# Kernel optimization log

Hardware: AMD Instinct MI355X
Metric: run time of the kernel (lower is better)

The kernel has to match this reference:

```python
import jax, jax.numpy as jnp
import numpy as np

B, V, P, L, D = 8, 16, 128, 16, 128
PD = L * D  # patch_dim = patch_size * d_model = 2048


def _layernorm(x, g, b, eps=1e-5):
    mu = jnp.mean(x, axis=-1, keepdims=True)
    var = jnp.mean(jnp.square(x - mu), axis=-1, keepdims=True)
    return (x - mu) / jnp.sqrt(var + eps) * g + b


def setup_inputs() -> dict:
    key = jax.random.key(0)
    ks = jax.random.split(key, 24)
    x = jax.random.normal(ks[0], (B, V, P, L, D), jnp.float32)
    m = jax.random.randint(ks[1], (B, V, V), 0, 2) > 0
    var_mask = m & ~jnp.eye(V, dtype=bool)[None]  # keep self-attention unmasked

    def lin_w(k, fan_in, fan_out):
        return jax.random.normal(k, (fan_in, fan_out), jnp.float32) * (1.0 / np.sqrt(fan_in))

    inp = {"x": x, "var_mask": var_mask}
    # Attn_PatchLevel (attn1): query / shared kv / out projections
    inp["w_q1"] = lin_w(ks[2], PD, PD); inp["b_q1"] = jnp.zeros((PD,), jnp.float32)
    inp["w_kv1"] = lin_w(ks[3], PD, PD); inp["b_kv1"] = jnp.zeros((PD,), jnp.float32)
    inp["w_o1"] = lin_w(ks[4], PD, PD); inp["b_o1"] = jnp.zeros((PD,), jnp.float32)
    # Attn_VarLevel (attn2)
    inp["w_q2"] = lin_w(ks[5], PD, PD); inp["b_q2"] = jnp.zeros((PD,), jnp.float32)
    inp["w_kv2"] = lin_w(ks[6], PD, PD); inp["b_kv2"] = jnp.zeros((PD,), jnp.float32)
    inp["w_o2"] = lin_w(ks[7], PD, PD); inp["b_o2"] = jnp.zeros((PD,), jnp.float32)
    # LayerNorms
    inp["g1"] = jnp.ones((PD,), jnp.float32); inp["be1"] = jnp.zeros((PD,), jnp.float32)
    inp["g2"] = jnp.ones((PD,), jnp.float32); inp["be2"] = jnp.zeros((PD,), jnp.float32)
    inp["g3"] = jnp.ones((PD,), jnp.float32); inp["be3"] = jnp.zeros((PD,), jnp.float32)
    # FFN
    inp["w_l1"] = lin_w(ks[8], PD, 4 * PD); inp["b_l1"] = jnp.zeros((4 * PD,), jnp.float32)
    inp["w_l2"] = lin_w(ks[9], 4 * PD, PD); inp["b_l2"] = jnp.zeros((PD,), jnp.float32)
    return inp


def reference(x, var_mask,
              w_q1, b_q1, w_kv1, b_kv1, w_o1, b_o1,
              w_q2, b_q2, w_kv2, b_kv2, w_o2, b_o2,
              g1, be1, g2, be2, g3, be3,
              w_l1, b_l1, w_l2, b_l2):
    b, v, p, l, d = x.shape
    pd = l * d
    scale = 1.0 / np.sqrt(pd)
    x = x.reshape(b, v, p, pd)

    # ---- Attn_PatchLevel (mask=None -> no masking; keys and values share kv_projection) ----
    q = x @ w_q1 + b_q1
    kv = x @ w_kv1 + b_kv1  # keys == values in the original module
    scores = jnp.einsum('bvpd,bvsd->bvps', q, kv)  # [B,V,P,P]
    attn = jax.nn.softmax(scale * scores, axis=-1)  # dropout is identity at eval
    a1 = jnp.einsum('bvps,bvsd->bvpd', attn, kv) @ w_o1 + b_o1
    x = _layernorm(x + a1, g1, be1)

    # ---- Attn_VarLevel over variables, per patch ----
    x = x.transpose(0, 2, 1, 3)  # [B,P,V,PD]
    q = x @ w_q2 + b_q2
    kv = x @ w_kv2 + b_kv2
    scores = jnp.einsum('bpvd,bprd->bpvr', q, kv)  # [B,P,V,V]
    scores = jnp.where(var_mask[:, None, :, :], -jnp.inf, scores)
    attn = jax.nn.softmax(scale * scores, axis=-1)
    a2 = jnp.einsum('bpvr,bprd->bpvd', attn, kv) @ w_o2 + b_o2
    x = _layernorm(x + a2, g2, be2)

    # ---- FFN (torch nn.GELU default = exact erf) ----
    z = jax.nn.gelu(x @ w_l1 + b_l1, approximate=False)
    x = x + z @ w_l2 + b_l2

    x_out = _layernorm(x, g3, be3).transpose(0, 2, 1, 3)  # [B,V,P,PD]
    x_next = x_out.reshape(b, v, p // 2, 2 * l, d)
    return x_out, x_next
```

## Files before the change

### kernel.cpp

```cpp
#include <hip/hip_runtime.h>
#include <math.h>


using u16   = unsigned short;
using f32x4 = __attribute__((ext_vector_type(4))) float;
using bf16x8= __attribute__((ext_vector_type(8))) __bf16;
using u16x8 = __attribute__((ext_vector_type(8))) u16;
using u16x4 = __attribute__((ext_vector_type(4))) u16;

#define NROWS 16384
#define PD    2048

__device__ __forceinline__ float bf2f(u16 u) {
    unsigned v = ((unsigned)u) << 16;
    return __builtin_bit_cast(float, v);
}
__device__ __forceinline__ u16 f2bf(float f) {
    unsigned u = __builtin_bit_cast(unsigned, f);
    u += 0x7FFFu + ((u >> 16) & 1u);
    return (u16)(u >> 16);
}
__device__ __forceinline__ void gload_lds16(const void* g, void* l) {
    __builtin_amdgcn_global_load_lds((const __attribute__((address_space(1))) void*)g,
                                     (__attribute__((address_space(3))) void*)l, 16, 0, 0);
}

template<int OUTF32, int GELU, int HASBIAS>
__global__ __launch_bounds__(256, 2)
void gemm_nt(const u16* __restrict__ A, long sAg, int lda,
             const u16* __restrict__ B, long sBg, int ldb,
             void* __restrict__ Cv, long sCg, int ldc,
             const float* __restrict__ bias, int K, float scale)
{
    __shared__ __align__(16) u16 lsA[128 * 32];
    __shared__ __align__(16) u16 lsB[128 * 32];

    const int tid  = threadIdx.x;
    const int w    = tid >> 6;
    const int lane = tid & 63;
    const int m0   = blockIdx.x * 128;
    const int n0   = blockIdx.y * 128;
    A += (long)blockIdx.z * sAg;
    B += (long)blockIdx.z * sBg;

    const int wr = w >> 1, wc = w & 1;

    f32x4 acc[4][4] = {};

    const int srow = lane >> 2;
    const int skc  = (lane & 3) * 8;
    const int rA0  = 32 * w + srow;
    const int rA1  = rA0 + 16;
    const size_t aoff0 = (size_t)(m0 + rA0) * lda + skc;
    const size_t aoff1 = (size_t)(m0 + rA1) * lda + skc;
    const size_t boff0 = (size_t)(n0 + rA0) * ldb + skc;
    const size_t boff1 = (size_t)(n0 + rA1) * ldb + skc;
    u16* lA0 = lsA + 1024 * w;
    u16* lA1 = lA0 + 512;
    u16* lB0 = lsB + 1024 * w;
    u16* lB1 = lB0 + 512;

    const int fr = lane & 15;
    const int fk = (lane >> 4) * 8;

    for (int k0 = 0; k0 < K; k0 += 32) {
        gload_lds16(A + aoff0 + k0, lA0);
        gload_lds16(A + aoff1 + k0, lA1);
        gload_lds16(B + boff0 + k0, lB0);
        gload_lds16(B + boff1 + k0, lB1);
        __syncthreads();

        bf16x8 af[4], bf[4];
        #pragma unroll
        for (int m = 0; m < 4; m++)
            af[m] = *(const bf16x8*)&lsA[(wr * 64 + m * 16 + fr) * 32 + fk];
        #pragma unroll
        for (int n = 0; n < 4; n++)
            bf[n] = *(const bf16x8*)&lsB[(wc * 64 + n * 16 + fr) * 32 + fk];
        #pragma unroll
        for (int m = 0; m < 4; m++)
            #pragma unroll
            for (int n = 0; n < 4; n++)
                acc[m][n] = __builtin_amdgcn_mfma_f32_16x16x32_bf16(af[m], bf[n], acc[m][n], 0, 0, 0);
        __syncthreads();
    }

    float* Cf = (float*)Cv;
    u16*   Cb = (u16*)Cv;
    const int crow0 = m0 + wr * 64 + (lane >> 4) * 4;
    const int ccol0 = n0 + wc * 64 + fr;
    const long cbase = (long)blockIdx.z * sCg;
    #pragma unroll
    for (int n = 0; n < 4; n++) {
        const int col = ccol0 + n * 16;
        float bb = 0.f;
        if constexpr (HASBIAS) bb = bias[col];
        #pragma unroll
        for (int m = 0; m < 4; m++) {
            #pragma unroll
            for (int j = 0; j < 4; j++) {
                const int row = crow0 + m * 16 + j;
                float v = acc[m][n][j] + bb;
                if constexpr (GELU) v = 0.5f * v * (1.f + erff(v * 0.70710678118f));
                const long idx = cbase + (long)row * ldc + col;
                if constexpr (OUTF32) Cf[idx] = v * scale;
                else                  Cb[idx] = f2bf(v);
            }
        }
    }
}

__global__ __launch_bounds__(256)
void wtrans_kernel(const float* __restrict__ in, u16* __restrict__ out, int R, int C)
{
    __shared__ float tile[32][33];
    const int c0 = blockIdx.x * 32, r0 = blockIdx.y * 32;
    const int tx = threadIdx.x & 31, ty = threadIdx.x >> 5;
    #pragma unroll
    for (int i = ty; i < 32; i += 8)
        tile[i][tx] = in[(size_t)(r0 + i) * C + c0 + tx];
    __syncthreads();
    #pragma unroll
    for (int i = ty; i < 32; i += 8)
        out[(size_t)(c0 + i) * R + r0 + tx] = f2bf(tile[tx][i]);
}

__global__ __launch_bounds__(256)
void kvtrans_kernel(const u16* __restrict__ in, u16* __restrict__ out)
{
    __shared__ u16 tile[32][33];
    const int g = blockIdx.z;
    const int n0 = blockIdx.x * 32, m0 = blockIdx.y * 32;
    const int tx = threadIdx.x & 31, ty = threadIdx.x >> 5;
    #pragma unroll
    for (int i = ty; i < 32; i += 8)
        tile[i][tx] = in[(size_t)(g * 128 + m0 + i) * 2048 + n0 + tx];
    __syncthreads();
    #pragma unroll
    for (int i = ty; i < 32; i += 8)
        out[(size_t)g * 262144 + (size_t)(n0 + i) * 128 + m0 + tx] = tile[tx][i];
}

__global__ __launch_bounds__(256)
void cvt_f32_bf16(const float* __restrict__ in, u16* __restrict__ out)
{
    const long i = ((long)blockIdx.x * 256 + threadIdx.x) * 4;
    float4 v = *(const float4*)(in + i);
    u16x4 o;
    o[0] = f2bf(v.x); o[1] = f2bf(v.y); o[2] = f2bf(v.z); o[3] = f2bf(v.w);
    *(u16x4*)(out + i) = o;
}

template<int FINAL>
__global__ __launch_bounds__(256)
void ln_kernel(const float* __restrict__ resid, const u16* __restrict__ add,
               const float* __restrict__ gam, const float* __restrict__ bet,
               u16* __restrict__ xb, float* __restrict__ o1, float* __restrict__ o2)
{
    const long row = blockIdx.x;
    const int  t   = threadIdx.x;
    const long base = row * PD + t * 8;

    u16x8  av = *(const u16x8*)(add + base);
    float4 r0 = *(const float4*)(resid + base);
    float4 r1 = *(const float4*)(resid + base + 4);
    float y[8];
    y[0] = r0.x + bf2f(av[0]); y[1] = r0.y + bf2f(av[1]);
    y[2] = r0.z + bf2f(av[2]); y[3] = r0.w + bf2f(av[3]);
    y[4] = r1.x + bf2f(av[4]); y[5] = r1.y + bf2f(av[5]);
    y[6] = r1.z + bf2f(av[6]); y[7] = r1.w + bf2f(av[7]);

    float s1 = 0.f, s2 = 0.f;
    #pragma unroll
    for (int j = 0; j < 8; j++) { s1 += y[j]; s2 += y[j] * y[j]; }
    #pragma unroll
    for (int d = 1; d < 64; d <<= 1) { s1 += __shfl_xor(s1, d); s2 += __shfl_xor(s2, d); }
    __shared__ float red[8];
    const int w = t >> 6;
    if ((t & 63) == 0) { red[w] = s1; red[4 + w] = s2; }
    __syncthreads();
    s1 = red[0] + red[1] + red[2] + red[3];
    s2 = red[4] + red[5] + red[6] + red[7];
    const float mean = s1 * (1.f / PD);
    const float var  = s2 * (1.f / PD) - mean * mean;
    const float rstd = rsqrtf(var + 1e-5f);

    float4 g0 = *(const float4*)(gam + t * 8);
    float4 g1 = *(const float4*)(gam + t * 8 + 4);
    float4 b0 = *(const float4*)(bet + t * 8);
    float4 b1 = *(const float4*)(bet + t * 8 + 4);
    float gv[8] = {g0.x, g0.y, g0.z, g0.w, g1.x, g1.y, g1.z, g1.w};
    float bv[8] = {b0.x, b0.y, b0.z, b0.w, b1.x, b1.y, b1.z, b1.w};

    float o[8];
    #pragma unroll
    for (int j = 0; j < 8; j++) o[j] = (y[j] - mean) * rstd * gv[j] + bv[j];

    if constexpr (FINAL) {
        float4 p0 = {o[0], o[1], o[2], o[3]}, p1 = {o[4], o[5], o[6], o[7]};
        *(float4*)(o1 + base) = p0; *(float4*)(o1 + base + 4) = p1;
        *(float4*)(o2 + base) = p0; *(float4*)(o2 + base + 4) = p1;
    } else {
        u16x8 ob;
        #pragma unroll
        for (int j = 0; j < 8; j++) ob[j] = f2bf(o[j]);
        *(u16x8*)(xb + base) = ob;
        float4 p0 = {o[0], o[1], o[2], o[3]}, p1 = {o[4], o[5], o[6], o[7]};
        *(float4*)(o1 + base) = p0; *(float4*)(o1 + base + 4) = p1;
    }
}

__global__ __launch_bounds__(256)
void softmax128_kernel(const float* __restrict__ S, u16* __restrict__ P)
{
    const int row  = blockIdx.x * 4 + (threadIdx.x >> 6);
    const int lane = threadIdx.x & 63;
    const float2 v = *(const float2*)(S + (size_t)row * 128 + lane * 2);
    float mx = fmaxf(v.x, v.y);
    #pragma unroll
    for (int d = 1; d < 64; d <<= 1) mx = fmaxf(mx, __shfl_xor(mx, d));
    const float e0 = __expf(v.x - mx), e1 = __expf(v.y - mx);
    float sm = e0 + e1;
    #pragma unroll
    for (int d = 1; d < 64; d <<= 1) sm += __shfl_xor(sm, d);
    const float inv = 1.f / sm;
    unsigned o = (unsigned)f2bf(e0 * inv) | ((unsigned)f2bf(e1 * inv) << 16);
    *(unsigned*)(P + (size_t)row * 128 + lane * 2) = o;
}

__global__ void detect_mask_kernel(const unsigned char* __restrict__ m, int* __restrict__ flag)
{
    __shared__ int s;
    if (threadIdx.x == 0) s = 0;
    __syncthreads();
    int acc = 0;
    for (int i = threadIdx.x; i < 2048; i += 256)
        if (i & 3) acc |= m[i];
    if (acc) atomicOr(&s, 1);
    __syncthreads();
    if (threadIdx.x == 0) *flag = s;
}

__global__ __launch_bounds__(64)
void attn2_kernel(u16* __restrict__ Q, const u16* __restrict__ KV,
                  const void* __restrict__ mask, const int* __restrict__ mflag,
                  float scale)
{
    const int g = blockIdx.x;
    const int b = g >> 7, p = g & 127;
    const int lane = threadIdx.x;

    const size_t groupbase = ((size_t)(b * 16) * 128 + p) * PD;
    const size_t vstride   = (size_t)128 * PD;

    const int am   = lane & 15;
    const int koff = (lane >> 4) * 8;
    const u16* qp = Q  + groupbase + (size_t)am * vstride + koff;
    const u16* kp = KV + groupbase + (size_t)am * vstride + koff;

    f32x4 acc = {0.f, 0.f, 0.f, 0.f};
    for (int k0 = 0; k0 < PD; k0 += 32) {
        bf16x8 a  = *(const bf16x8*)(qp + k0);
        bf16x8 bb = *(const bf16x8*)(kp + k0);
        acc = __builtin_amdgcn_mfma_f32_16x16x32_bf16(a, bb, acc, 0, 0, 0);
    }

    const int vk = lane & 15;
    const int hi = lane >> 4;
    const int mf = *mflag;
    __shared__ float PL[16][16];
    float pv[4];
    #pragma unroll
    for (int j = 0; j < 4; j++) {
        const int vq = hi * 4 + j;
        float s = acc[j] * scale;
        const int midx = b * 256 + vq * 16 + vk;
        int msk;
        if (mf) msk = ((const unsigned char*)mask)[midx];
        else    msk = ((const int*)mask)[midx];
        if (msk) s = -1e30f;
        pv[j] = s;
    }
    #pragma unroll
    for (int j = 0; j < 4; j++) {
        float mx = pv[j];
        #pragma unroll
        for (int d = 1; d < 16; d <<= 1) mx = fmaxf(mx, __shfl_xor(mx, d));
        const float e = __expf(pv[j] - mx);
        float sm = e;
        #pragma unroll
        for (int d = 1; d < 16; d <<= 1) sm += __shfl_xor(sm, d);
        pv[j] = e / sm;
    }
    #pragma unroll
    for (int j = 0; j < 4; j++) PL[hi * 4 + j][vk] = pv[j];
    __syncthreads();

    const u16* kvr[16];
    #pragma unroll
    for (int v = 0; v < 16; v++) kvr[v] = KV + groupbase + (size_t)v * vstride;

    for (int vqt = 0; vqt < 16; vqt += 4) {
        float pr[4][16];
        #pragma unroll
        for (int q = 0; q < 4; q++)
            #pragma unroll
            for (int k = 0; k < 16; k++) pr[q][k] = PL[vqt + q][k];
        u16* o0 = Q + groupbase + (size_t)(vqt + 0) * vstride;
        u16* o1 = Q + groupbase + (size_t)(vqt + 1) * vstride;
        u16* o2 = Q + groupbase + (size_t)(vqt + 2) * vstride;
        u16* o3 = Q + groupbase + (size_t)(vqt + 3) * vstride;
        for (int n0 = 0; n0 < PD; n0 += 64) {
            const int n = n0 + lane;
            float a0 = 0.f, a1 = 0.f, a2 = 0.f, a3 = 0.f;
            #pragma unroll
            for (int k = 0; k < 16; k++) {
                const float kvv = bf2f(kvr[k][n]);
                a0 += pr[0][k] * kvv; a1 += pr[1][k] * kvv;
                a2 += pr[2][k] * kvv; a3 += pr[3][k] * kvv;
            }
            o0[n] = f2bf(a0); o1[n] = f2bf(a1); o2[n] = f2bf(a2); o3[n] = f2bf(a3);
        }
    }
}

extern "C" void kernel_launch(void* const* d_in, const int* in_sizes, int n_in,
                              void* d_out, int out_size, void* d_ws, size_t ws_size,
                              hipStream_t stream)
{
    const float* x0    = (const float*)d_in[0];
    const void*  vmask = d_in[1];
    const float* w_q1  = (const float*)d_in[2];  const float* b_q1  = (const float*)d_in[3];
    const float* w_kv1 = (const float*)d_in[4];  const float* b_kv1 = (const float*)d_in[5];
    const float* w_o1  = (const float*)d_in[6];  const float* b_o1  = (const float*)d_in[7];
    const float* w_q2  = (const float*)d_in[8];  const float* b_q2  = (const float*)d_in[9];
    const float* w_kv2 = (const float*)d_in[10]; const float* b_kv2 = (const float*)d_in[11];
    const float* w_o2  = (const float*)d_in[12]; const float* b_o2  = (const float*)d_in[13];
    const float* g1 = (const float*)d_in[14]; const float* be1 = (const float*)d_in[15];
    const float* g2 = (const float*)d_in[16]; const float* be2 = (const float*)d_in[17];
    const float* g3 = (const float*)d_in[18]; const float* be3 = (const float*)d_in[19];
    const float* w_l1 = (const float*)d_in[20]; const float* b_l1 = (const float*)d_in[21];
    const float* w_l2 = (const float*)d_in[22]; const float* b_l2 = (const float*)d_in[23];

    char* ws = (char*)d_ws;
    size_t off = 0;
    auto alloc = [&](size_t bytes) { size_t o = off; off += (bytes + 255) & ~(size_t)255; return o; };
    const size_t oWQ1  = alloc(8388608),  oWKV1 = alloc(8388608),  oWO1 = alloc(8388608);
    const size_t oWQ2  = alloc(8388608),  oWKV2 = alloc(8388608),  oWO2 = alloc(8388608);
    const size_t oWL1  = alloc(33554432), oWL2  = alloc(33554432);
    const size_t oXB   = alloc(67108864);
    const size_t oQ    = alloc(67108864);
    const size_t oKV   = alloc(67108864);
    const size_t oKVT  = alloc(67108864);
    const size_t oR    = alloc(134217728);
    const size_t oS    = alloc(8388608);
    const size_t oP1   = alloc(4194304);
    const size_t oFLAG = alloc(256);
    if (ws_size < off) return;

    u16* WQ1T = (u16*)(ws + oWQ1);  u16* WKV1T = (u16*)(ws + oWKV1); u16* WO1T = (u16*)(ws + oWO1);
    u16* WQ2T = (u16*)(ws + oWQ2);  u16* WKV2T = (u16*)(ws + oWKV2); u16* WO2T = (u16*)(ws + oWO2);
    u16* WL1T = (u16*)(ws + oWL1);  u16* WL2T  = (u16*)(ws + oWL2);
    u16* XB   = (u16*)(ws + oXB);   u16* Q     = (u16*)(ws + oQ);
    u16* KV   = (u16*)(ws + oKV);   u16* KVT   = (u16*)(ws + oKVT);
    float* R  = (float*)(ws + oR);  float* S   = (float*)(ws + oS);
    u16* P1   = (u16*)(ws + oP1);   int* FLAG  = (int*)(ws + oFLAG);

    const float scale = 0.02209708691f;
    float* out0 = (float*)d_out;
    float* out1 = out0 + (size_t)NROWS * PD;

    detect_mask_kernel<<<1, 256, 0, stream>>>((const unsigned char*)vmask, FLAG);

    wtrans_kernel<<<dim3(64, 64), 256, 0, stream>>>(w_q1,  WQ1T,  2048, 2048);
    wtrans_kernel<<<dim3(64, 64), 256, 0, stream>>>(w_kv1, WKV1T, 2048, 2048);
    wtrans_kernel<<<dim3(64, 64), 256, 0, stream>>>(w_o1,  WO1T,  2048, 2048);
    wtrans_kernel<<<dim3(64, 64), 256, 0, stream>>>(w_q2,  WQ2T,  2048, 2048);
    wtrans_kernel<<<dim3(64, 64), 256, 0, stream>>>(w_kv2, WKV2T, 2048, 2048);
    wtrans_kernel<<<dim3(64, 64), 256, 0, stream>>>(w_o2,  WO2T,  2048, 2048);
    wtrans_kernel<<<dim3(256, 64), 256, 0, stream>>>(w_l1, WL1T, 2048, 8192);
    wtrans_kernel<<<dim3(64, 256), 256, 0, stream>>>(w_l2, WL2T, 8192, 2048);

    cvt_f32_bf16<<<32768, 256, 0, stream>>>(x0, XB);

    gemm_nt<0,0,1><<<dim3(128,16,1), 256, 0, stream>>>(XB, 0, 2048, WQ1T,  0, 2048, Q,  0, 2048, b_q1,  2048, 1.f);
    gemm_nt<0,0,1><<<dim3(128,16,1), 256, 0, stream>>>(XB, 0, 2048, WKV1T, 0, 2048, KV, 0, 2048, b_kv1, 2048, 1.f);
    kvtrans_kernel<<<dim3(64, 4, 128), 256, 0, stream>>>(KV, KVT);
    gemm_nt<1,0,0><<<dim3(1,1,128), 256, 0, stream>>>(Q, 262144, 2048, KV, 262144, 2048, S, 16384, 128, nullptr, 2048, scale);
    softmax128_kernel<<<4096, 256, 0, stream>>>(S, P1);
    gemm_nt<0,0,0><<<dim3(1,16,128), 256, 0, stream>>>(P1, 16384, 128, KVT, 262144, 128, Q, 262144, 2048, nullptr, 128, 1.f);
    gemm_nt<0,0,1><<<dim3(128,16,1), 256, 0, stream>>>(Q, 0, 2048, WO1T, 0, 2048, KV, 0, 2048, b_o1, 2048, 1.f);
    ln_kernel<0><<<NROWS, 256, 0, stream>>>(x0, KV, g1, be1, XB, R, nullptr);

    gemm_nt<0,0,1><<<dim3(128,16,1), 256, 0, stream>>>(XB, 0, 2048, WQ2T,  0, 2048, Q,  0, 2048, b_q2,  2048, 1.f);
    gemm_nt<0,0,1><<<dim3(128,16,1), 256, 0, stream>>>(XB, 0, 2048, WKV2T, 0, 2048, KV, 0, 2048, b_kv2, 2048, 1.f);
    attn2_kernel<<<1024, 64, 0, stream>>>(Q, KV, vmask, FLAG, scale);
    gemm_nt<0,0,1><<<dim3(128,16,1), 256, 0, stream>>>(Q, 0, 2048, WO2T, 0, 2048, KV, 0, 2048, b_o2, 2048, 1.f);
    ln_kernel<0><<<NROWS, 256, 0, stream>>>(R, KV, g2, be2, XB, R, nullptr);

    for (int c = 0; c < 4; c++) {
        const long rows = (long)c * 4096;
        gemm_nt<0,1,1><<<dim3(32,64,1), 256, 0, stream>>>(XB + rows * 2048, 0, 2048, WL1T, 0, 2048, Q, 0, 8192, b_l1, 2048, 1.f);
        gemm_nt<0,0,1><<<dim3(32,16,1), 256, 0, stream>>>(Q, 0, 8192, WL2T, 0, 8192, KV + rows * 2048, 0, 2048, b_l2, 8192, 1.f);
    }
    ln_kernel<1><<<NROWS, 256, 0, stream>>>(R, KV, g3, be3, nullptr, out0, out1);
}
```

Baseline: 2.980 ms.

## Add 256x256 tiled bf16 GEMM with double-buffered LDS and use for projections/FFN

Introduces a new 512-thread GEMM kernel with 256x256 output tiles, a 64-wide K step, XOR-swizzled LDS and direct global-to-LDS loads. It double-buffers the K stages, interleaves loads with MFMA quarters under s_setprio, and remaps workgroups in a grouped order for L2 reuse. All large projection and FFN GEMMs switch to it, and the FFN is processed in two 8192-row chunks instead of four. The aim is higher MFMA utilisation and less global traffic per FLOP, at the cost of 128KB of LDS per block and lower occupancy.

```diff
diff --git a/kernel.cpp b/kernel.cpp
--- a/kernel.cpp
+++ b/kernel.cpp
@@ -25,7 +25,171 @@
                                      (__attribute__((address_space(3))) void*)l, 16, 0, 0);
 }
 
-template<int OUTF32, int GELU, int HASBIAS>
+template<int GELU>
+__global__ __launch_bounds__(512, 2)
+void gemm256(const u16* __restrict__ A, int lda,
+             const u16* __restrict__ B, int ldb,
+             u16* __restrict__ C, int ldc,
+             const float* __restrict__ bias, int K)
+{
+    __shared__ __align__(16) char smem[131072];
+
+    const int tid  = threadIdx.x;
+    const int wv   = tid >> 6;
+    const int wm   = wv >> 2;
+    const int wn   = wv & 3;
+    const int lane = tid & 63;
+    const int fr   = lane & 15;
+    const int fks16= (lane >> 4) * 16;
+    const int rmask= (fr & 7) << 4;
+    const int kb0  = fks16 ^ rmask;
+    const int kb1  = (64 + fks16) ^ rmask;
+
+    const int gx = gridDim.x, gy = gridDim.y;
+    const int nwg = gx * gy;
+    int flat = blockIdx.x * gy + blockIdx.y;
+    flat = (flat & 7) * (nwg >> 3) + (flat >> 3);
+    const int m0 = (flat / gy) * 256;
+    const int n0 = (flat % gy) * 256;
+
+    const int rsub = tid >> 3;
+    const int cswE = (((tid & 7) * 16) ^ ((rsub & 7) << 4)) >> 1;
+    const int waveByte = wv * 1024;
+
+    auto stage = [&](const u16* mat, int ld, int row0, int k0, int regionByte) {
+        const u16* g0 = mat + (size_t)(row0 + rsub) * ld + k0 + cswE;
+        gload_lds16(g0,               smem + regionByte + waveByte);
+        gload_lds16(g0 + (size_t)ld * 64, smem + regionByte + 8192 + waveByte);
+    };
+
+    const int aRowByte = (wm * 128 + fr) * 128;
+    const int bRowByte = (wn * 64 + fr) * 128;
+
+    const int KT = K >> 6;
+
+    stage(A, lda, m0,       0, 0);
+    stage(B, ldb, n0,       0, 32768);
+    stage(A, lda, m0 + 128, 0, 16384);
+    stage(B, ldb, n0 + 128, 0, 49152);
+    stage(B, ldb, n0,      64, 98304);
+    stage(A, lda, m0,      64, 65536);
+    asm volatile("s_waitcnt vmcnt(4)" ::: "memory");
+    __builtin_amdgcn_s_barrier();
+
+    bf16x8 a[4][2], b0[2][2], b1[2][2];
+    f32x4  acc[8][4] = {};
+
+    for (int t = 0; t < KT; ++t) {
+        const int Ab = (t & 1) ? 65536 : 0;
+        const int Bb = Ab + 32768;
+        const int Ob = Ab ^ 65536;
+        const bool s1 = (t + 1 < KT), s2 = (t + 2 < KT);
+
+        #pragma unroll
+        for (int mi = 0; mi < 4; ++mi) {
+            const int rb = Ab + aRowByte + mi * 2048;
+            a[mi][0] = *(const bf16x8*)(smem + rb + kb0);
+            a[mi][1] = *(const bf16x8*)(smem + rb + kb1);
+        }
+        #pragma unroll
+        for (int nj = 0; nj < 2; ++nj) {
+            const int rb = Bb + bRowByte + nj * 2048;
+            b0[nj][0] = *(const bf16x8*)(smem + rb + kb0);
+            b0[nj][1] = *(const bf16x8*)(smem + rb + kb1);
+        }
+        if (s1) stage(B, ldb, n0 + 128, (t + 1) << 6, Ob + 49152);
+        __builtin_amdgcn_s_barrier();
+        asm volatile("s_waitcnt lgkmcnt(0)" ::: "memory");
+        __builtin_amdgcn_sched_barrier(0);
+        __builtin_amdgcn_s_setprio(1);
+        #pragma unroll
+        for (int mi = 0; mi < 4; ++mi)
+            #pragma unroll
+            for (int nj = 0; nj < 2; ++nj) {
+                acc[mi][nj] = __builtin_amdgcn_mfma_f32_16x16x32_bf16(a[mi][0], b0[nj][0], acc[mi][nj], 0, 0, 0);
+                acc[mi][nj] = __builtin_amdgcn_mfma_f32_16x16x32_bf16(a[mi][1], b0[nj][1], acc[mi][nj], 0, 0, 0);
+            }
+        __builtin_amdgcn_s_setprio(0);
+        __builtin_amdgcn_s_barrier();
+
+        #pragma unroll
+        for (int nj = 0; nj < 2; ++nj) {
+            const int rb = Bb + bRowByte + 4096 + nj * 2048;
+            b1[nj][0] = *(const bf16x8*)(smem + rb + kb0);
+            b1[nj][1] = *(const bf16x8*)(smem + rb + kb1);
+        }
+        if (s1) stage(A, lda, m0 + 128, (t + 1) << 6, Ob + 16384);
+        __builtin_amdgcn_s_barrier();
+        asm volatile("s_waitcnt lgkmcnt(0)" ::: "memory");
+        __builtin_amdgcn_sched_barrier(0);
+        __builtin_amdgcn_s_setprio(1);
+        #pragma unroll
+        for (int mi = 0; mi < 4; ++mi)
+            #pragma unroll
+            for (int nj = 0; nj < 2; ++nj) {
+                acc[mi][2 + nj] = __builtin_amdgcn_mfma_f32_16x16x32_bf16(a[mi][0], b1[nj][0], acc[mi][2 + nj], 0, 0, 0);
+                acc[mi][2 + nj] = __builtin_amdgcn_mfma_f32_16x16x32_bf16(a[mi][1], b1[nj][1], acc[mi][2 + nj], 0, 0, 0);
+            }
+        __builtin_amdgcn_s_setprio(0);
+        __builtin_amdgcn_s_barrier();
+
+        #pragma unroll
+        for (int mi = 0; mi < 4; ++mi) {
+            const int rb = Ab + aRowByte + 8192 + mi * 2048;
+            a[mi][0] = *(const bf16x8*)(smem + rb + kb0);
+            a[mi][1] = *(const bf16x8*)(smem + rb + kb1);
+        }
+        if (s2) stage(B, ldb, n0, (t + 2) << 6, Bb);
+        __builtin_amdgcn_s_barrier();
+        asm volatile("s_waitcnt lgkmcnt(0)" ::: "memory");
+        __builtin_amdgcn_sched_barrier(0);
+        __builtin_amdgcn_s_setprio(1);
+        #pragma unroll
+        for (int mi = 0; mi < 4; ++mi)
+            #pragma unroll
+            for (int nj = 0; nj < 2; ++nj) {
+                acc[4 + mi][nj] = __builtin_amdgcn_mfma_f32_16x16x32_bf16(a[mi][0], b0[nj][0], acc[4 + mi][nj], 0, 0, 0);
+                acc[4 + mi][nj] = __builtin_amdgcn_mfma_f32_16x16x32_bf16(a[mi][1], b0[nj][1], acc[4 + mi][nj], 0, 0, 0);
+            }
+        __builtin_amdgcn_s_setprio(0);
+        __builtin_amdgcn_s_barrier();
+
+        if (s2) stage(A, lda, m0, (t + 2) << 6, Ab);
+        __builtin_amdgcn_s_barrier();
+        __builtin_amdgcn_s_setprio(1);
+        #pragma unroll
+        for (int mi = 0; mi < 4; ++mi)
+            #pragma unroll
+            for (int nj = 0; nj < 2; ++nj) {
+                acc[4 + mi][2 + nj] = __builtin_amdgcn_mfma_f32_16x16x32_bf16(a[mi][0], b1[nj][0], acc[4 + mi][2 + nj], 0, 0, 0);
+                acc[4 + mi][2 + nj] = __builtin_amdgcn_mfma_f32_16x16x32_bf16(a[mi][1], b1[nj][1], acc[4 + mi][2 + nj], 0, 0, 0);
+            }
+        __builtin_amdgcn_s_setprio(0);
+        if (s2) { asm volatile("s_waitcnt vmcnt(4)" ::: "memory"); }
+        else    { asm volatile("s_waitcnt vmcnt(0)" ::: "memory"); }
+        __builtin_amdgcn_s_barrier();
+    }
+
+    const int colBase = n0 + wn * 64 + fr;
+    const int rowBase = m0 + wm * 128 + (lane >> 4) * 4;
+    #pragma unroll
+    for (int nj = 0; nj < 4; ++nj) {
+        const int col = colBase + nj * 16;
+        const float bb = bias[col];
+        #pragma unroll
+        for (int mi = 0; mi < 8; ++mi) {
+            #pragma unroll
+            for (int j = 0; j < 4; ++j) {
+                const int row = rowBase + mi * 16 + j;
+                float v = acc[mi][nj][j] + bb;
+                if constexpr (GELU) v = 0.5f * v * (1.f + erff(v * 0.70710678118f));
+                C[(size_t)row * ldc + col] = f2bf(v);
+            }
+        }
+    }
+}
+
+template<int OUTF32, int HASBIAS>
 __global__ __launch_bounds__(256, 2)
 void gemm_nt(const u16* __restrict__ A, long sAg, int lda,
              const u16* __restrict__ B, long sBg, int ldb,
@@ -44,7 +208,6 @@
     B += (long)blockIdx.z * sBg;
 
     const int wr = w >> 1, wc = w & 1;
-
     f32x4 acc[4][4] = {};
 
     const int srow = lane >> 2;
@@ -101,7 +264,6 @@
             for (int j = 0; j < 4; j++) {
                 const int row = crow0 + m * 16 + j;
                 float v = acc[m][n][j] + bb;
-                if constexpr (GELU) v = 0.5f * v * (1.f + erff(v * 0.70710678118f));
                 const long idx = cbase + (long)row * ldc + col;
                 if constexpr (OUTF32) Cf[idx] = v * scale;
                 else                  Cb[idx] = f2bf(v);
@@ -330,12 +492,18 @@
 {
     const float* x0    = (const float*)d_in[0];
     const void*  vmask = d_in[1];
-    const float* w_q1  = (const float*)d_in[2];  const float* b_q1  = (const float*)d_in[3];
-    const float* w_kv1 = (const float*)d_in[4];  const float* b_kv1 = (const float*)d_in[5];
-    const float* w_o1  = (const float*)d_in[6];  const float* b_o1  = (const float*)d_in[7];
-    const float* w_q2  = (const float*)d_in[8];  const float* b_q2  = (const float*)d_in[9];
-    const float* w_kv2 = (const float*)d_in[10]; const float* b_kv2 = (const float*)d_in[11];
-    const float* w_o2  = (const float*)d_in[12]; const float* b_o2  = (const float*)d_in[13];
+    const float* b_q1  = (const float*)d_in[3];
+    const float* b_kv1 = (const float*)d_in[5];
+    const float* b_o1  = (const float*)d_in[7];
+    const float* b_q2  = (const float*)d_in[9];
+    const float* b_kv2 = (const float*)d_in[11];
+    const float* b_o2  = (const float*)d_in[13];
+    const float* w_q1  = (const float*)d_in[2];
+    const float* w_kv1 = (const float*)d_in[4];
+    const float* w_o1  = (const float*)d_in[6];
+    const float* w_q2  = (const float*)d_in[8];
+    const float* w_kv2 = (const float*)d_in[10];
+    const float* w_o2  = (const float*)d_in[12];
     const float* g1 = (const float*)d_in[14]; const float* be1 = (const float*)d_in[15];
     const float* g2 = (const float*)d_in[16]; const float* be2 = (const float*)d_in[17];
     const float* g3 = (const float*)d_in[18]; const float* be3 = (const float*)d_in[19];
@@ -365,6 +533,8 @@
     u16* KV   = (u16*)(ws + oKV);   u16* KVT   = (u16*)(ws + oKVT);
     float* R  = (float*)(ws + oR);  float* S   = (float*)(ws + oS);
     u16* P1   = (u16*)(ws + oP1);   int* FLAG  = (int*)(ws + oFLAG);
+    u16* H    = Q;
+    u16* F    = KVT;
 
     const float scale = 0.02209708691f;
     float* out0 = (float*)d_out;
@@ -383,25 +553,25 @@
 
     cvt_f32_bf16<<<32768, 256, 0, stream>>>(x0, XB);
 
-    gemm_nt<0,0,1><<<dim3(128,16,1), 256, 0, stream>>>(XB, 0, 2048, WQ1T,  0, 2048, Q,  0, 2048, b_q1,  2048, 1.f);
-    gemm_nt<0,0,1><<<dim3(128,16,1), 256, 0, stream>>>(XB, 0, 2048, WKV1T, 0, 2048, KV, 0, 2048, b_kv1, 2048, 1.f);
+    gemm256<0><<<dim3(64, 8), 512, 0, stream>>>(XB, 2048, WQ1T,  2048, Q,  2048, b_q1,  2048);
+    gemm256<0><<<dim3(64, 8), 512, 0, stream>>>(XB, 2048, WKV1T, 2048, KV, 2048, b_kv1, 2048);
     kvtrans_kernel<<<dim3(64, 4, 128), 256, 0, stream>>>(KV, KVT);
-    gemm_nt<1,0,0><<<dim3(1,1,128), 256, 0, stream>>>(Q, 262144, 2048, KV, 262144, 2048, S, 16384, 128, nullptr, 2048, scale);
+    gemm_nt<1,0><<<dim3(1,1,128), 256, 0, stream>>>(Q, 262144, 2048, KV, 262144, 2048, S, 16384, 128, nullptr, 2048, scale);
     softmax128_kernel<<<4096, 256, 0, stream>>>(S, P1);
-    gemm_nt<0,0,0><<<dim3(1,16,128), 256, 0, stream>>>(P1, 16384, 128, KVT, 262144, 128, Q, 262144, 2048, nullptr, 128, 1.f);
-    gemm_nt<0,0,1><<<dim3(128,16,1), 256, 0, stream>>>(Q, 0, 2048, WO1T, 0, 2048, KV, 0, 2048, b_o1, 2048, 1.f);
+    gemm_nt<0,0><<<dim3(1,16,128), 256, 0, stream>>>(P1, 16384, 128, KVT, 262144, 128, Q, 262144, 2048, nullptr, 128, 1.f);
+    gemm256<0><<<dim3(64, 8), 512, 0, stream>>>(Q, 2048, WO1T, 2048, KV, 2048, b_o1, 2048);
     ln_kernel<0><<<NROWS, 256, 0, stream>>>(x0, KV, g1, be1, XB, R, nullptr);
 
-    gemm_nt<0,0,1><<<dim3(128,16,1), 256, 0, stream>>>(XB, 0, 2048, WQ2T,  0, 2048, Q,  0, 2048, b_q2,  2048, 1.f);
-    gemm_nt<0,0,1><<<dim3(128,16,1), 256, 0, stream>>>(XB, 0, 2048, WKV2T, 0, 2048, KV, 0, 2048, b_kv2, 2048, 1.f);
+    gemm256<0><<<dim3(64, 8), 512, 0, stream>>>(XB, 2048, WQ2T,  2048, Q,  2048, b_q2,  2048);
+    gemm256<0><<<dim3(64, 8), 512, 0, stream>>>(XB, 2048, WKV2T, 2048, KV, 2048, b_kv2, 2048);
     attn2_kernel<<<1024, 64, 0, stream>>>(Q, KV, vmask, FLAG, scale);
-    gemm_nt<0,0,1><<<dim3(128,16,1), 256, 0, stream>>>(Q, 0, 2048, WO2T, 0, 2048, KV, 0, 2048, b_o2, 2048, 1.f);
+    gemm256<0><<<dim3(64, 8), 512, 0, stream>>>(Q, 2048, WO2T, 2048, KV, 2048, b_o2, 2048);
     ln_kernel<0><<<NROWS, 256, 0, stream>>>(R, KV, g2, be2, XB, R, nullptr);
 
-    for (int c = 0; c < 4; c++) {
-        const long rows = (long)c * 4096;
-        gemm_nt<0,1,1><<<dim3(32,64,1), 256, 0, stream>>>(XB + rows * 2048, 0, 2048, WL1T, 0, 2048, Q, 0, 8192, b_l1, 2048, 1.f);
-        gemm_nt<0,0,1><<<dim3(32,16,1), 256, 0, stream>>>(Q, 0, 8192, WL2T, 0, 8192, KV + rows * 2048, 0, 2048, b_l2, 8192, 1.f);
-    }
-    ln_kernel<1><<<NROWS, 256, 0, stream>>>(R, KV, g3, be3, nullptr, out0, out1);
-}
+    for (int c = 0; c < 2; c++) {
+        const size_t rows = (size_t)c * 8192;
+        gemm256<1><<<dim3(32, 32), 512, 0, stream>>>(XB + rows * 2048, 2048, WL1T, 2048, H, 8192, b_l1, 2048);
+        gemm256<0><<<dim3(32, 8),  512, 0, stream>>>(H, 8192, WL2T, 8192, F + rows * 2048, 2048, b_l2, 8192);
+    }
+    ln_kernel<1><<<NROWS, 256, 0, stream>>>(R, F, g3, be3, nullptr, out0, out1);
+}
```

Measured after the change: 2.612 ms. 1.14x faster.
